# Kernel tuning notes

Measured on AMD Instinct MI355X. Metric: run time of the kernel, lower is better.

The kernel has to match this reference:

```python
import jax, jax.numpy as jnp
import numpy as np

B = 524288          # batch
C = 128             # num_classes
CONF_PEN = 0.5      # confusion_penalty coefficient
PROB_THRESH = 0.2   # wrong-prob threshold from original loop
WEIGHT_THRESH = 1.0 # weight threshold from original loop


def setup_inputs() -> dict:
    key = jax.random.key(0)
    k1, k2, k3 = jax.random.split(key, 3)
    # scale logits so softmax is peaky enough that the >0.2 branch fires
    outputs = 5.0 * jax.random.normal(k1, (B, C), dtype=jnp.float32)
    labels = jax.random.randint(k2, (B,), 0, C, dtype=jnp.int32)
    # uniform in [0, 2): roughly half the weights exceed the 1.0 threshold
    confusion_weights = jax.random.uniform(k3, (C, C), dtype=jnp.float32, minval=0.0, maxval=2.0)
    return {"outputs": outputs, "labels": labels, "confusion_weights": confusion_weights}


def reference(outputs, labels, confusion_weights):
    # base cross-entropy (mean over batch), numerically stable
    logp = jax.nn.log_softmax(outputs, axis=-1)                       # [B, C]
    base_loss = -jnp.take_along_axis(logp, labels[:, None].astype(jnp.int32), axis=1).mean()

    # confusion penalty (computed under no_grad in the original)
    probs = jnp.exp(logp)                                             # [B, C]
    w = confusion_weights[labels]                                     # [B, C] row per true label
    cls = jnp.arange(outputs.shape[1])
    mask = (cls[None, :] != labels[:, None]) & (w > WEIGHT_THRESH) & (probs > PROB_THRESH)
    pen_sum = jnp.sum(jnp.where(mask, w * probs, jnp.float32(0.0)))
    count = jnp.sum(mask)
    penalty = jnp.where(count > 0, pen_sum / jnp.maximum(count, 1).astype(pen_sum.dtype), jnp.float32(0.0))
    penalty = jax.lax.stop_gradient(penalty)  # mirrors torch.no_grad block

    return base_loss + CONF_PEN * penalty
```

## Files before the change

kernel.cpp:

```cpp
#include <hip/hip_runtime.h>

#define B_ROWS 524288
#define C_CLS  128
#define CONF_PEN 0.5f
#define PROB_THRESH 0.2f
#define WEIGHT_THRESH 1.0f

#define BLOCKS 2048
#define THREADS 256
#define WAVES_PER_BLOCK (THREADS / 64)
#define PAIRS 4
#define NWAVES (BLOCKS * WAVES_PER_BLOCK)
#define ROWS_PER_SWEEP (NWAVES * 2 * PAIRS)
#define ITERS (B_ROWS / ROWS_PER_SWEEP)

template <int CTRL>
__device__ __forceinline__ float dpp_add(float x) {
    int y = __builtin_amdgcn_update_dpp(0, __float_as_int(x), CTRL, 0xF, 0xF, true);
    return x + __int_as_float(y);
}

__device__ __forceinline__ float sum32(float s) {
    s = dpp_add<0xB1>(s);
    s = dpp_add<0x4E>(s);
    s = dpp_add<0x141>(s);
    s = dpp_add<0x140>(s);
    s += __shfl_xor(s, 16);
    return s;
}

__global__ __launch_bounds__(THREADS, 4) void afl_main(
    const float* __restrict__ outputs,
    const int* __restrict__ labels,
    const float* __restrict__ cw,
    float* __restrict__ partial) {

    const int lane = threadIdx.x & 63;
    const int wave = threadIdx.x >> 6;
    const int half = lane >> 5;
    const int sub  = lane & 31;
    const int gwave = blockIdx.x * WAVES_PER_BLOCK + wave;

    float base_acc = 0.0f;
    float pen_acc  = 0.0f;
    float cnt_acc  = 0.0f;

    const int row0 = gwave * (2 * PAIRS);

    #pragma unroll 2
    for (int it = 0; it < ITERS; ++it) {
        const int base = row0 + it * ROWS_PER_SWEEP;

        float4 v[PAIRS];
        int    lab[PAIRS];
        float4 w[PAIRS];

        #pragma unroll
        for (int j = 0; j < PAIRS; ++j) {
            const int row = base + 2 * j + half;
            v[j]   = ((const float4*)(outputs + (size_t)row * C_CLS))[sub];
            lab[j] = labels[row];
        }
        #pragma unroll
        for (int j = 0; j < PAIRS; ++j) {
            w[j] = ((const float4*)(cw + (size_t)lab[j] * C_CLS))[sub];
        }

        float e0[PAIRS], e1[PAIRS], e2[PAIRS], e3[PAIRS], s[PAIRS];
        #pragma unroll
        for (int j = 0; j < PAIRS; ++j) {
            e0[j] = __expf(v[j].x);
            e1[j] = __expf(v[j].y);
            e2[j] = __expf(v[j].z);
            e3[j] = __expf(v[j].w);
            s[j]  = (e0[j] + e1[j]) + (e2[j] + e3[j]);
        }

        #pragma unroll
        for (int j = 0; j < PAIRS; ++j)
            s[j] = sum32(s[j]);

        #pragma unroll
        for (int j = 0; j < PAIRS; ++j) {
            const float logZ  = __logf(s[j]);
            const float inv_s = 1.0f / s[j];

            if ((lab[j] >> 2) == sub) {
                const float xl = (lab[j] & 2) ? ((lab[j] & 1) ? v[j].w : v[j].z)
                                              : ((lab[j] & 1) ? v[j].y : v[j].x);
                base_acc += logZ - xl;
            }

            const int c0 = 4 * sub;
            float p;
            p = e0[j] * inv_s;
            if (c0 + 0 != lab[j] && w[j].x > WEIGHT_THRESH && p > PROB_THRESH) { pen_acc += w[j].x * p; cnt_acc += 1.0f; }
            p = e1[j] * inv_s;
            if (c0 + 1 != lab[j] && w[j].y > WEIGHT_THRESH && p > PROB_THRESH) { pen_acc += w[j].y * p; cnt_acc += 1.0f; }
            p = e2[j] * inv_s;
            if (c0 + 2 != lab[j] && w[j].z > WEIGHT_THRESH && p > PROB_THRESH) { pen_acc += w[j].z * p; cnt_acc += 1.0f; }
            p = e3[j] * inv_s;
            if (c0 + 3 != lab[j] && w[j].w > WEIGHT_THRESH && p > PROB_THRESH) { pen_acc += w[j].w * p; cnt_acc += 1.0f; }
        }
    }

    #pragma unroll
    for (int off = 32; off >= 1; off >>= 1) {
        base_acc += __shfl_xor(base_acc, off);
        pen_acc  += __shfl_xor(pen_acc, off);
        cnt_acc  += __shfl_xor(cnt_acc, off);
    }

    __shared__ float s_base[WAVES_PER_BLOCK];
    __shared__ float s_pen [WAVES_PER_BLOCK];
    __shared__ float s_cnt [WAVES_PER_BLOCK];
    if (lane == 0) {
        s_base[wave] = base_acc;
        s_pen [wave] = pen_acc;
        s_cnt [wave] = cnt_acc;
    }
    __syncthreads();
    if (threadIdx.x == 0) {
        float b = 0.0f, pn = 0.0f, c = 0.0f;
        #pragma unroll
        for (int i = 0; i < WAVES_PER_BLOCK; ++i) {
            b += s_base[i]; pn += s_pen[i]; c += s_cnt[i];
        }
        partial[3 * blockIdx.x + 0] = b;
        partial[3 * blockIdx.x + 1] = pn;
        partial[3 * blockIdx.x + 2] = c;
    }
}

__global__ __launch_bounds__(256) void afl_finalize(
    const float* __restrict__ partial, float* __restrict__ out) {
    float b = 0.0f, pn = 0.0f, c = 0.0f;
    for (int i = threadIdx.x; i < BLOCKS; i += 256) {
        b  += partial[3 * i + 0];
        pn += partial[3 * i + 1];
        c  += partial[3 * i + 2];
    }
    #pragma unroll
    for (int off = 32; off >= 1; off >>= 1) {
        b  += __shfl_xor(b, off);
        pn += __shfl_xor(pn, off);
        c  += __shfl_xor(c, off);
    }
    __shared__ float sb[4], sp[4], sc[4];
    const int wave = threadIdx.x >> 6;
    if ((threadIdx.x & 63) == 0) { sb[wave] = b; sp[wave] = pn; sc[wave] = c; }
    __syncthreads();
    if (threadIdx.x == 0) {
        b  = sb[0] + sb[1] + sb[2] + sb[3];
        pn = sp[0] + sp[1] + sp[2] + sp[3];
        c  = sc[0] + sc[1] + sc[2] + sc[3];
        const float penalty = (c > 0.0f) ? (pn / c) : 0.0f;
        out[0] = b * (1.0f / (float)B_ROWS) + CONF_PEN * penalty;
    }
}

extern "C" void kernel_launch(void* const* d_in, const int* in_sizes, int n_in,
                              void* d_out, int out_size, void* d_ws, size_t ws_size,
                              hipStream_t stream) {
    const float* outputs = (const float*)d_in[0];
    const int*   labels  = (const int*)d_in[1];
    const float* cw      = (const float*)d_in[2];
    float* out = (float*)d_out;
    float* partial = (float*)d_ws;

    afl_main<<<BLOCKS, THREADS, 0, stream>>>(outputs, labels, cw, partial);
    afl_finalize<<<1, 256, 0, stream>>>(partial, out);
}
```

Before: 360.7 us.

## Prefetch next rows in registers and premask confusion weights in prep kernel

Adds a small prep kernel that zeros confusion weights on the diagonal or at or below the threshold, so the main loop can drop the label and weight comparisons. The main loop now software-pipelines its loads: logits for the next sweep and labels two sweeps ahead are fetched while the current sweep is computed. The probability threshold is compared on unnormalized exponentials, and the penalty sum is built with branchless FMAs using a hardware reciprocal. This costs an extra kernel launch and more registers, and the occupancy hint drops from 4 to 3 blocks per CU.

```diff
diff --git a/kernel.cpp b/kernel.cpp
--- a/kernel.cpp
+++ b/kernel.cpp
@@ -8,18 +8,17 @@
 
 #define BLOCKS 2048
 #define THREADS 256
-#define WAVES_PER_BLOCK (THREADS / 64)
+#define WPB (THREADS / 64)
 #define PAIRS 4
-#define NWAVES (BLOCKS * WAVES_PER_BLOCK)
-#define ROWS_PER_SWEEP (NWAVES * 2 * PAIRS)
-#define ITERS (B_ROWS / ROWS_PER_SWEEP)
+#define NWAVES (BLOCKS * WPB)
+#define SWEEP (NWAVES * 2 * PAIRS)
+#define ITERS (B_ROWS / SWEEP)
 
 template <int CTRL>
 __device__ __forceinline__ float dpp_add(float x) {
     int y = __builtin_amdgcn_update_dpp(0, __float_as_int(x), CTRL, 0xF, 0xF, true);
     return x + __int_as_float(y);
 }
-
 __device__ __forceinline__ float sum32(float s) {
     s = dpp_add<0xB1>(s);
     s = dpp_add<0x4E>(s);
@@ -29,78 +28,101 @@
     return s;
 }
 
-__global__ __launch_bounds__(THREADS, 4) void afl_main(
+__global__ __launch_bounds__(THREADS) void afl_prep(
+    const float* __restrict__ cw, float* __restrict__ cwp) {
+    const int i = blockIdx.x * THREADS + threadIdx.x;
+    const int r = i >> 7, c = i & 127;
+    const float w = cw[i];
+    cwp[i] = (c != r && w > WEIGHT_THRESH) ? w : 0.0f;
+}
+
+__global__ __launch_bounds__(THREADS, 3) void afl_main(
     const float* __restrict__ outputs,
     const int* __restrict__ labels,
-    const float* __restrict__ cw,
+    const float* __restrict__ cwp,
     float* __restrict__ partial) {
 
     const int lane = threadIdx.x & 63;
     const int wave = threadIdx.x >> 6;
     const int half = lane >> 5;
     const int sub  = lane & 31;
-    const int gwave = blockIdx.x * WAVES_PER_BLOCK + wave;
+    const int gwave = blockIdx.x * WPB + wave;
+    const int row0  = gwave * (2 * PAIRS);
 
-    float base_acc = 0.0f;
-    float pen_acc  = 0.0f;
-    float cnt_acc  = 0.0f;
+    float base_acc = 0.0f, pen_acc = 0.0f, cnt_acc = 0.0f;
 
-    const int row0 = gwave * (2 * PAIRS);
+    int    labc[PAIRS], labn[PAIRS];
+    float4 vc[PAIRS];
+    #pragma unroll
+    for (int j = 0; j < PAIRS; ++j)
+        labc[j] = labels[row0 + 2 * j + half];
+    #pragma unroll
+    for (int j = 0; j < PAIRS; ++j)
+        labn[j] = labels[row0 + SWEEP + 2 * j + half];
+    #pragma unroll
+    for (int j = 0; j < PAIRS; ++j)
+        vc[j] = ((const float4*)(outputs + (size_t)(row0 + 2 * j + half) * C_CLS))[sub];
 
-    #pragma unroll 2
     for (int it = 0; it < ITERS; ++it) {
-        const int base = row0 + it * ROWS_PER_SWEEP;
+        const int base = row0 + it * SWEEP;
 
-        float4 v[PAIRS];
-        int    lab[PAIRS];
         float4 w[PAIRS];
+        #pragma unroll
+        for (int j = 0; j < PAIRS; ++j)
+            w[j] = ((const float4*)(cwp + (size_t)labc[j] * C_CLS))[sub];
+
+        float4 vn[PAIRS];
+        int    lab2[PAIRS];
+        if (it + 1 < ITERS) {
+            #pragma unroll
+            for (int j = 0; j < PAIRS; ++j)
+                vn[j] = ((const float4*)(outputs + (size_t)(base + SWEEP + 2 * j + half) * C_CLS))[sub];
+        }
+        if (it + 2 < ITERS) {
+            #pragma unroll
+            for (int j = 0; j < PAIRS; ++j)
+                lab2[j] = labels[base + 2 * SWEEP + 2 * j + half];
+        }
 
         #pragma unroll
         for (int j = 0; j < PAIRS; ++j) {
-            const int row = base + 2 * j + half;
-            v[j]   = ((const float4*)(outputs + (size_t)row * C_CLS))[sub];
-            lab[j] = labels[row];
-        }
-        #pragma unroll
-        for (int j = 0; j < PAIRS; ++j) {
-            w[j] = ((const float4*)(cw + (size_t)lab[j] * C_CLS))[sub];
-        }
+            const float e0 = __expf(vc[j].x);
+            const float e1 = __expf(vc[j].y);
+            const float e2 = __expf(vc[j].z);
+            const float e3 = __expf(vc[j].w);
+            float s = (e0 + e1) + (e2 + e3);
+            s = sum32(s);
 
-        float e0[PAIRS], e1[PAIRS], e2[PAIRS], e3[PAIRS], s[PAIRS];
-        #pragma unroll
-        for (int j = 0; j < PAIRS; ++j) {
-            e0[j] = __expf(v[j].x);
-            e1[j] = __expf(v[j].y);
-            e2[j] = __expf(v[j].z);
-            e3[j] = __expf(v[j].w);
-            s[j]  = (e0[j] + e1[j]) + (e2[j] + e3[j]);
-        }
+            const float thr   = PROB_THRESH * s;
+            const float inv_s = __builtin_amdgcn_rcpf(s);
+            const float logZ  = __logf(s);
 
-        #pragma unroll
-        for (int j = 0; j < PAIRS; ++j)
-            s[j] = sum32(s[j]);
-
-        #pragma unroll
-        for (int j = 0; j < PAIRS; ++j) {
-            const float logZ  = __logf(s[j]);
-            const float inv_s = 1.0f / s[j];
-
-            if ((lab[j] >> 2) == sub) {
-                const float xl = (lab[j] & 2) ? ((lab[j] & 1) ? v[j].w : v[j].z)
-                                              : ((lab[j] & 1) ? v[j].y : v[j].x);
+            if ((labc[j] >> 2) == sub) {
+                const float xl = (labc[j] & 2) ? ((labc[j] & 1) ? vc[j].w : vc[j].z)
+                                               : ((labc[j] & 1) ? vc[j].y : vc[j].x);
                 base_acc += logZ - xl;
             }
 
-            const int c0 = 4 * sub;
-            float p;
-            p = e0[j] * inv_s;
-            if (c0 + 0 != lab[j] && w[j].x > WEIGHT_THRESH && p > PROB_THRESH) { pen_acc += w[j].x * p; cnt_acc += 1.0f; }
-            p = e1[j] * inv_s;
-            if (c0 + 1 != lab[j] && w[j].y > WEIGHT_THRESH && p > PROB_THRESH) { pen_acc += w[j].y * p; cnt_acc += 1.0f; }
-            p = e2[j] * inv_s;
-            if (c0 + 2 != lab[j] && w[j].z > WEIGHT_THRESH && p > PROB_THRESH) { pen_acc += w[j].z * p; cnt_acc += 1.0f; }
-            p = e3[j] * inv_s;
-            if (c0 + 3 != lab[j] && w[j].w > WEIGHT_THRESH && p > PROB_THRESH) { pen_acc += w[j].w * p; cnt_acc += 1.0f; }
+            float ps = 0.0f;
+            ps = fmaf(w[j].x, (e0 > thr) ? e0 : 0.0f, ps);
+            ps = fmaf(w[j].y, (e1 > thr) ? e1 : 0.0f, ps);
+            ps = fmaf(w[j].z, (e2 > thr) ? e2 : 0.0f, ps);
+            ps = fmaf(w[j].w, (e3 > thr) ? e3 : 0.0f, ps);
+            pen_acc = fmaf(ps, inv_s, pen_acc);
+
+            cnt_acc += ((w[j].x != 0.0f) && (e0 > thr)) ? 1.0f : 0.0f;
+            cnt_acc += ((w[j].y != 0.0f) && (e1 > thr)) ? 1.0f : 0.0f;
+            cnt_acc += ((w[j].z != 0.0f) && (e2 > thr)) ? 1.0f : 0.0f;
+            cnt_acc += ((w[j].w != 0.0f) && (e3 > thr)) ? 1.0f : 0.0f;
+        }
+
+        if (it + 1 < ITERS) {
+            #pragma unroll
+            for (int j = 0; j < PAIRS; ++j) { vc[j] = vn[j]; labc[j] = labn[j]; }
+            if (it + 2 < ITERS) {
+                #pragma unroll
+                for (int j = 0; j < PAIRS; ++j) labn[j] = lab2[j];
+            }
         }
     }
 
@@ -111,21 +133,13 @@
         cnt_acc  += __shfl_xor(cnt_acc, off);
     }
 
-    __shared__ float s_base[WAVES_PER_BLOCK];
-    __shared__ float s_pen [WAVES_PER_BLOCK];
-    __shared__ float s_cnt [WAVES_PER_BLOCK];
-    if (lane == 0) {
-        s_base[wave] = base_acc;
-        s_pen [wave] = pen_acc;
-        s_cnt [wave] = cnt_acc;
-    }
+    __shared__ float s_base[WPB], s_pen[WPB], s_cnt[WPB];
+    if (lane == 0) { s_base[wave] = base_acc; s_pen[wave] = pen_acc; s_cnt[wave] = cnt_acc; }
     __syncthreads();
     if (threadIdx.x == 0) {
         float b = 0.0f, pn = 0.0f, c = 0.0f;
         #pragma unroll
-        for (int i = 0; i < WAVES_PER_BLOCK; ++i) {
-            b += s_base[i]; pn += s_pen[i]; c += s_cnt[i];
-        }
+        for (int i = 0; i < WPB; ++i) { b += s_base[i]; pn += s_pen[i]; c += s_cnt[i]; }
         partial[3 * blockIdx.x + 0] = b;
         partial[3 * blockIdx.x + 1] = pn;
         partial[3 * blockIdx.x + 2] = c;
@@ -165,9 +179,11 @@
     const float* outputs = (const float*)d_in[0];
     const int*   labels  = (const int*)d_in[1];
     const float* cw      = (const float*)d_in[2];
-    float* out = (float*)d_out;
+    float* out     = (float*)d_out;
     float* partial = (float*)d_ws;
+    float* cwp     = (float*)d_ws + 16384;
 
-    afl_main<<<BLOCKS, THREADS, 0, stream>>>(outputs, labels, cw, partial);
+    afl_prep<<<(C_CLS * C_CLS) / THREADS, THREADS, 0, stream>>>(cw, cwp);
+    afl_main<<<BLOCKS, THREADS, 0, stream>>>(outputs, labels, cwp, partial);
     afl_finalize<<<1, 256, 0, stream>>>(partial, out);
 }
```

Measured after the change: 360.5 us. About the same (-0.1%).
